# Optimization experiments

Hardware: AMD Instinct MI355X
Metric: run time of the kernel (lower is better)

Reference implementation:

```python
import jax, jax.numpy as jnp
import numpy as np

NEG_SLOPE = 0.2
N_NODES = 50000


def gat_conv(x, src, dst, W, a_src, a_dst, b, n_nodes):
    """One PyG-style GATConv layer (eval mode, self-loops already in src/dst).
    x: [N, F_in]; W: [F_in, H*C]; a_src/a_dst: [H, C]; b: [H*C] or [C].
    Returns per-node, per-head outputs [N, H, C].
    """
    H, C = a_src.shape
    h = (x @ W).reshape(-1, H, C)                      # [N, H, C]
    s_src = jnp.sum(h * a_src[None], axis=-1)          # [N, H]
    s_dst = jnp.sum(h * a_dst[None], axis=-1)          # [N, H]
    e = jax.nn.leaky_relu(s_src[src] + s_dst[dst], NEG_SLOPE)   # [E, H]
    # segment softmax over incoming edges of each destination node
    m = jax.ops.segment_max(e, dst, num_segments=n_nodes)       # [N, H]
    w = jnp.exp(e - m[dst])                                     # [E, H]
    denom = jax.ops.segment_sum(w, dst, num_segments=n_nodes)   # [N, H]
    alpha = w / denom[dst]                                      # [E, H]
    # weighted aggregation of source features
    out = jax.ops.segment_sum(alpha[:, :, None] * h[src], dst, num_segments=n_nodes)
    return out  # [N, H, C]


def setup_inputs() -> dict:
    key = jax.random.key(0)
    ks = jax.random.split(key, 12)
    N, F_in, Hid, H, F_out = N_NODES, 128, 64, 4, 128
    E = 800000
    x = jax.random.normal(ks[0], (N, F_in), dtype=jnp.float32)
    edge_index = jax.random.randint(ks[1], (2, E), 0, N, dtype=jnp.int64)
    sc = 0.1
    return {
        "x": x,
        "edge_index": edge_index,
        "W1": jax.random.normal(ks[2], (F_in, H * Hid), dtype=jnp.float32) * sc,
        "att_src1": jax.random.normal(ks[3], (H, Hid), dtype=jnp.float32) * sc,
        "att_dst1": jax.random.normal(ks[4], (H, Hid), dtype=jnp.float32) * sc,
        "b1": jnp.zeros((H * Hid,), dtype=jnp.float32),
        "W2": jax.random.normal(ks[5], (H * Hid, F_out), dtype=jnp.float32) * sc,
        "att_src2": jax.random.normal(ks[6], (1, F_out), dtype=jnp.float32) * sc,
        "att_dst2": jax.random.normal(ks[7], (1, F_out), dtype=jnp.float32) * sc,
        "b2": jnp.zeros((F_out,), dtype=jnp.float32),
    }


def reference(x, edge_index, W1, att_src1, att_dst1, b1, W2, att_src2, att_dst2, b2):
    N = x.shape[0]
    # PyG GATConv adds self-loops by default
    loops = jnp.arange(N, dtype=edge_index.dtype)
    src = jnp.concatenate([edge_index[0], loops])
    dst = jnp.concatenate([edge_index[1], loops])
    # layer 1: heads=4, concat -> [N, H*Hid], then ELU (dropout is identity in eval)
    h1 = gat_conv(x, src, dst, W1, att_src1, att_dst1, b1, N)    # [N, H, Hid]
    h1 = h1.reshape(N, -1) + b1
    h1 = jax.nn.elu(h1)
    # layer 2: heads=1, concat=False -> mean over the single head
    h2 = gat_conv(h1, src, dst, W2, att_src2, att_dst2, b2, N)   # [N, 1, F_out]
    out = h2[:, 0, :] + b2
    return out
```

## Files before the change

### kernel.cpp

```cpp
#include <hip/hip_runtime.h>
#include <cmath>

typedef __attribute__((ext_vector_type(8))) short bf16x8;
typedef __attribute__((ext_vector_type(4))) float f32x4;

static __device__ __forceinline__ unsigned short f2bf(float f) {
    unsigned u = __float_as_uint(f);
    unsigned r = (u + 0x7fffu + ((u >> 16) & 1u)) >> 16;
    return (unsigned short)r;
}
static __device__ __forceinline__ unsigned packbf(float a, float b) {
    return (unsigned)f2bf(a) | ((unsigned)f2bf(b) << 16);
}
static __device__ __forceinline__ float bflo(unsigned u) { return __uint_as_float(u << 16); }
static __device__ __forceinline__ float bfhi(unsigned u) { return __uint_as_float(u & 0xffff0000u); }

__global__ void prep_k(const float* __restrict__ x, const float* __restrict__ W1,
                       const float* __restrict__ W2, const int* __restrict__ dst,
                       unsigned* __restrict__ xb,
                       unsigned short* __restrict__ Wt1, unsigned short* __restrict__ Wt2,
                       int* __restrict__ deg, int NX2, int NW1, int NW2, int E) {
    int i = blockIdx.x * blockDim.x + threadIdx.x;
    if (i < NX2) {
        float2 v = reinterpret_cast<const float2*>(x)[i];
        xb[i] = packbf(v.x, v.y);
        return;
    }
    i -= NX2;
    if (i < NW1) { int nn = i / 128, k = i % 128; Wt1[i] = f2bf(W1[(size_t)k * 256 + nn]); return; }
    i -= NW1;
    if (i < NW2) { int nn = i / 256, k = i % 256; Wt2[i] = f2bf(W2[(size_t)k * 128 + nn]); return; }
    i -= NW2;
    if (i < E) atomicAdd(&deg[dst[i]], 1);
}

#define SCAN_BLK 256
#define SCAN_ELEMS 2048

__global__ void scan1_k(const int* __restrict__ deg, int* __restrict__ rowstart,
                        int* __restrict__ bsums, int N) {
    __shared__ int sh[SCAN_BLK];
    int t = threadIdx.x;
    int base = blockIdx.x * SCAN_ELEMS + t * 8;
    int vals[8];
    int sum = 0;
#pragma unroll
    for (int i = 0; i < 8; ++i) {
        int idx = base + i;
        vals[i] = (idx < N) ? (deg[idx] + 1) : 0;
        sum += vals[i];
    }
    sh[t] = sum;
    __syncthreads();
    for (int off = 1; off < SCAN_BLK; off <<= 1) {
        int v = (t >= off) ? sh[t - off] : 0;
        __syncthreads();
        sh[t] += v;
        __syncthreads();
    }
    int run = sh[t] - sum;
    if (t == SCAN_BLK - 1) bsums[blockIdx.x] = sh[t];
#pragma unroll
    for (int i = 0; i < 8; ++i) {
        int idx = base + i;
        if (idx < N) rowstart[idx] = run;
        run += vals[i];
    }
}
__global__ void scan2_k(int* __restrict__ bsums, int nb) {
    int lane = threadIdx.x;
    int own = (lane < nb) ? bsums[lane] : 0;
    int v = own;
    for (int off = 1; off < 64; off <<= 1) {
        int t = __shfl_up(v, off, 64);
        if (lane >= off) v += t;
    }
    if (lane < nb) bsums[lane] = v - own;
}
__global__ void scan3_init_k(int* __restrict__ rowstart, const int* __restrict__ bsums,
                             int* __restrict__ adj, int* __restrict__ cursor, int N, int total) {
    int i = blockIdx.x * blockDim.x + threadIdx.x;
    if (i < N) {
        int r = rowstart[i] + bsums[i / SCAN_ELEMS];
        rowstart[i] = r;
        adj[r] = i;
        cursor[i] = r + 1;
    } else if (i == N) {
        rowstart[N] = total;
    }
}
__global__ void scatter_k(const int* __restrict__ src, const int* __restrict__ dst, int E,
                          int* __restrict__ cursor, int* __restrict__ adj) {
    int e = blockIdx.x * blockDim.x + threadIdx.x;
    if (e >= E) return;
    int pos = atomicAdd(&cursor[dst[e]], 1);
    adj[pos] = src[e];
}

template<int K, int NOUT>
__global__ __launch_bounds__(256) void gemm_mfma_k(const unsigned* __restrict__ Ab,
                                                   const unsigned* __restrict__ Bt,
                                                   unsigned short* __restrict__ Yb, int N) {
    __shared__ unsigned short As[128 * 64];
    __shared__ unsigned short Bs[64 * 64];
    int tid = threadIdx.x;
    int lane = tid & 63, wid = tid >> 6;
    int wm = wid >> 1, wc = wid & 1;
    int m0 = blockIdx.x * 128;
    int n0 = blockIdx.y * 64;

    f32x4 acc[4][2] = {};

    for (int k0 = 0; k0 < K; k0 += 64) {
#pragma unroll
        for (int p = 0; p < 4; ++p) {
            int gl = p * 256 + tid;
            int row = gl >> 3, g = gl & 7;
            int grow = m0 + row; if (grow >= N) grow = N - 1;
            uint4 v = *reinterpret_cast<const uint4*>(Ab + (size_t)grow * (K / 2) + k0 / 2 + g * 4);
            *reinterpret_cast<uint4*>((char*)As + row * 128 + ((g ^ (row & 7)) << 4)) = v;
        }
#pragma unroll
        for (int p = 0; p < 2; ++p) {
            int gl = p * 256 + tid;
            int row = gl >> 3, g = gl & 7;
            uint4 v = *reinterpret_cast<const uint4*>(Bt + (size_t)(n0 + row) * (K / 2) + k0 / 2 + g * 4);
            *reinterpret_cast<uint4*>((char*)Bs + row * 128 + ((g ^ (row & 7)) << 4)) = v;
        }
        __syncthreads();

        bf16x8 bfrag[2][2];
#pragma unroll
        for (int kk = 0; kk < 2; ++kk)
#pragma unroll
            for (int no = 0; no < 2; ++no) {
                int row = wc * 32 + no * 16 + (lane & 15);
                int g = kk * 4 + (lane >> 4);
                bfrag[kk][no] = *reinterpret_cast<const bf16x8*>((char*)Bs + row * 128 + ((g ^ (row & 7)) << 4));
            }
#pragma unroll
        for (int mo = 0; mo < 4; ++mo) {
#pragma unroll
            for (int kk = 0; kk < 2; ++kk) {
                int row = wm * 64 + mo * 16 + (lane & 15);
                int g = kk * 4 + (lane >> 4);
                bf16x8 afrag = *reinterpret_cast<const bf16x8*>((char*)As + row * 128 + ((g ^ (row & 7)) << 4));
                acc[mo][0] = __builtin_amdgcn_mfma_f32_16x16x32_bf16(afrag, bfrag[kk][0], acc[mo][0], 0, 0, 0);
                acc[mo][1] = __builtin_amdgcn_mfma_f32_16x16x32_bf16(afrag, bfrag[kk][1], acc[mo][1], 0, 0, 0);
            }
        }
        __syncthreads();
    }
#pragma unroll
    for (int mo = 0; mo < 4; ++mo)
#pragma unroll
        for (int no = 0; no < 2; ++no) {
            int col = n0 + wc * 32 + no * 16 + (lane & 15);
            int rbase = m0 + wm * 64 + mo * 16 + (lane >> 4) * 4;
#pragma unroll
            for (int j = 0; j < 4; ++j) {
                int row = rbase + j;
                if (row < N) Yb[(size_t)row * NOUT + col] = f2bf(acc[mo][no][j]);
            }
        }
}

template<int H, int C>
__global__ void score_b_k(const unsigned* __restrict__ hb, const float* __restrict__ a_src,
                          const float* __restrict__ a_dst,
                          float* __restrict__ ssrc, float* __restrict__ sdst, int N) {
    int idx = blockIdx.x * blockDim.x + threadIdx.x;
    if (idx >= N * H) return;
    int n = idx / H, hh = idx % H;
    const uint4* hp = reinterpret_cast<const uint4*>(hb + (size_t)n * (H * C / 2) + hh * (C / 2));
    const float* as = a_src + hh * C;
    const float* ad = a_dst + hh * C;
    float ss = 0.f, sd = 0.f;
#pragma unroll
    for (int i = 0; i < C / 8; ++i) {
        uint4 u = hp[i];
        float v[8] = {bflo(u.x), bfhi(u.x), bflo(u.y), bfhi(u.y),
                      bflo(u.z), bfhi(u.z), bflo(u.w), bfhi(u.w)};
#pragma unroll
        for (int j = 0; j < 8; ++j) { ss += v[j] * as[i * 8 + j]; sd += v[j] * ad[i * 8 + j]; }
    }
    ssrc[idx] = ss;
    sdst[idx] = sd;
}

template<int H, int C, int GRP, bool ELU, bool OUT_BF16>
__global__ void node_agg_k(const int* __restrict__ rowstart, const int* __restrict__ adj,
                           const float* __restrict__ ssrc, const float* __restrict__ sdst,
                           const unsigned* __restrict__ hb, const float* __restrict__ bias,
                           void* __restrict__ outp, int N) {
    constexpr int HC = H * C;
    constexpr int ROW_U = HC / 2;
    constexpr int ULN = ROW_U / GRP;
    constexpr int FPLn = ULN * 2;
    constexpr int NGRP = 64 / GRP;
    int lane = threadIdx.x & 63;
    int w = threadIdx.x >> 6;
    int n = blockIdx.x * (blockDim.x >> 6) + w;
    if (n >= N) return;

    __shared__ int   s_sh[4][64];
    __shared__ float a_sh[4][64 * H];

    int r0 = rowstart[n], r1 = rowstart[n + 1];
    int deg = r1 - r0;

    float sd[H];
#pragma unroll
    for (int h = 0; h < H; ++h) sd[h] = sdst[n * H + h];

    if (deg <= 64) {
        int s = adj[r0 + ((lane < deg) ? lane : 0)];
        float a[H], l[H];
        {
            float v[H];
            if constexpr (H == 4) {
                float4 sv = reinterpret_cast<const float4*>(ssrc)[s];
                v[0] = sv.x; v[1] = sv.y; v[2] = sv.z; v[3] = sv.w;
            } else {
                v[0] = ssrc[s];
            }
#pragma unroll
            for (int h = 0; h < H; ++h) {
                float t = v[h] + sd[h];
                t = t > 0.f ? t : 0.2f * t;
                a[h] = (lane < deg) ? __expf(t) : 0.f;
                l[h] = a[h];
            }
            if (deg > 32)
#pragma unroll
                for (int h = 0; h < H; ++h) l[h] += __shfl_xor(l[h], 32, 64);
#pragma unroll
            for (int off = 16; off; off >>= 1)
#pragma unroll
                for (int h = 0; h < H; ++h) l[h] += __shfl_xor(l[h], off, 64);
#pragma unroll
            for (int h = 0; h < H; ++h) a[h] *= __builtin_amdgcn_rcpf(l[h]);
        }
        s_sh[w][lane] = s;
#pragma unroll
        for (int h = 0; h < H; ++h) a_sh[w][lane * H + h] = a[h];

        int g = lane / GRP, ln = lane % GRP;
        int hA = (ln * FPLn) / C;
        const unsigned* hbl = hb + ln * ULN;
        float acc[FPLn];
#pragma unroll
        for (int f = 0; f < FPLn; ++f) acc[f] = 0.f;

        int j = g;
        for (; j + 3 * NGRP < deg; j += 4 * NGRP) {
            int s0 = s_sh[w][j],            s1 = s_sh[w][j + NGRP];
            int s2 = s_sh[w][j + 2 * NGRP], s3 = s_sh[w][j + 3 * NGRP];
            float al0 = a_sh[w][j * H + hA],            al1 = a_sh[w][(j + NGRP) * H + hA];
            float al2 = a_sh[w][(j + 2 * NGRP) * H + hA], al3 = a_sh[w][(j + 3 * NGRP) * H + hA];
            uint4 u0 = *reinterpret_cast<const uint4*>(hbl + (size_t)s0 * ROW_U);
            uint4 u1 = *reinterpret_cast<const uint4*>(hbl + (size_t)s1 * ROW_U);
            uint4 u2 = *reinterpret_cast<const uint4*>(hbl + (size_t)s2 * ROW_U);
            uint4 u3 = *reinterpret_cast<const uint4*>(hbl + (size_t)s3 * ROW_U);
            acc[0] += al0 * bflo(u0.x); acc[1] += al0 * bfhi(u0.x);
            acc[2] += al0 * bflo(u0.y); acc[3] += al0 * bfhi(u0.y);
            acc[4] += al0 * bflo(u0.z); acc[5] += al0 * bfhi(u0.z);
            acc[6] += al0 * bflo(u0.w); acc[7] += al0 * bfhi(u0.w);
            acc[0] += al1 * bflo(u1.x); acc[1] += al1 * bfhi(u1.x);
            acc[2] += al1 * bflo(u1.y); acc[3] += al1 * bfhi(u1.y);
            acc[4] += al1 * bflo(u1.z); acc[5] += al1 * bfhi(u1.z);
            acc[6] += al1 * bflo(u1.w); acc[7] += al1 * bfhi(u1.w);
            acc[0] += al2 * bflo(u2.x); acc[1] += al2 * bfhi(u2.x);
            acc[2] += al2 * bflo(u2.y); acc[3] += al2 * bfhi(u2.y);
            acc[4] += al2 * bflo(u2.z); acc[5] += al2 * bfhi(u2.z);
            acc[6] += al2 * bflo(u2.w); acc[7] += al2 * bfhi(u2.w);
            acc[0] += al3 * bflo(u3.x); acc[1] += al3 * bfhi(u3.x);
            acc[2] += al3 * bflo(u3.y); acc[3] += al3 * bfhi(u3.y);
            acc[4] += al3 * bflo(u3.z); acc[5] += al3 * bfhi(u3.z);
            acc[6] += al3 * bflo(u3.w); acc[7] += al3 * bfhi(u3.w);
        }
        for (; j < deg; j += NGRP) {
            int sj = s_sh[w][j];
            float al = a_sh[w][j * H + hA];
            uint4 u = *reinterpret_cast<const uint4*>(hbl + (size_t)sj * ROW_U);
            acc[0] += al * bflo(u.x); acc[1] += al * bfhi(u.x);
            acc[2] += al * bflo(u.y); acc[3] += al * bfhi(u.y);
            acc[4] += al * bflo(u.z); acc[5] += al * bfhi(u.z);
            acc[6] += al * bflo(u.w); acc[7] += al * bfhi(u.w);
        }
#pragma unroll
        for (int off = GRP; off < 64; off <<= 1)
#pragma unroll
            for (int f = 0; f < FPLn; ++f) acc[f] += __shfl_xor(acc[f], off, 64);
#pragma unroll
        for (int f = 0; f < FPLn; ++f) {
            float v = acc[f] + bias[ln * FPLn + f];
            if (ELU) v = v > 0.f ? v : (__expf(v) - 1.f);
            acc[f] = v;
        }
        if (g == 0) {
            if constexpr (OUT_BF16) {
                unsigned* op = (unsigned*)outp + (size_t)n * ROW_U + ln * ULN;
                uint4 u = {packbf(acc[0], acc[1]), packbf(acc[2], acc[3]),
                           packbf(acc[4], acc[5]), packbf(acc[6], acc[7])};
                *reinterpret_cast<uint4*>(op) = u;
            } else {
                float* op = (float*)outp + (size_t)n * HC + ln * FPLn;
                *reinterpret_cast<float4*>(op) = make_float4(acc[0], acc[1], acc[2], acc[3]);
                *reinterpret_cast<float4*>(op + 4) = make_float4(acc[4], acc[5], acc[6], acc[7]);
            }
        }
    } else {
        constexpr int FPL = HC / 64;
        constexpr int UPL = FPL / 2;
        int hA = (lane * FPL) / C;
        float acc[FPL];
#pragma unroll
        for (int f = 0; f < FPL; ++f) acc[f] = 0.f;
        float m[H], l[H];
#pragma unroll
        for (int h = 0; h < H; ++h) { m[h] = -1e30f; l[h] = 0.f; }
        for (int e = r0 + lane; e < r1; e += 64) {
            int s = adj[e];
#pragma unroll
            for (int h = 0; h < H; ++h) {
                float v = ssrc[s * H + h] + sd[h];
                v = v > 0.f ? v : 0.2f * v;
                float mn = fmaxf(m[h], v);
                l[h] = l[h] * __expf(m[h] - mn) + __expf(v - mn);
                m[h] = mn;
            }
        }
#pragma unroll
        for (int off = 32; off; off >>= 1)
#pragma unroll
            for (int h = 0; h < H; ++h) {
                float mo = __shfl_xor(m[h], off, 64);
                float lo = __shfl_xor(l[h], off, 64);
                float mn = fmaxf(m[h], mo);
                l[h] = l[h] * __expf(m[h] - mn) + lo * __expf(mo - mn);
                m[h] = mn;
            }
        float mh = m[hA], invl = 1.f / l[hA], sdh = sd[hA];
        for (int e = r0; e < r1; ++e) {
            int s = adj[e];
            float v = ssrc[s * H + hA] + sdh;
            v = v > 0.f ? v : 0.2f * v;
            float alpha = __expf(v - mh) * invl;
            const unsigned* hp = hb + (size_t)s * ROW_U + lane * UPL;
            if constexpr (UPL == 2) {
                uint2 u = *reinterpret_cast<const uint2*>(hp);
                acc[0] += alpha * bflo(u.x); acc[1] += alpha * bfhi(u.x);
                acc[2] += alpha * bflo(u.y); acc[3] += alpha * bfhi(u.y);
            } else {
                unsigned u = *hp;
                acc[0] += alpha * bflo(u); acc[1] += alpha * bfhi(u);
            }
        }
#pragma unroll
        for (int f = 0; f < FPL; ++f) {
            float v = acc[f] + bias[lane * FPL + f];
            if (ELU) v = v > 0.f ? v : (__expf(v) - 1.f);
            acc[f] = v;
        }
        if constexpr (OUT_BF16) {
            unsigned* op = (unsigned*)outp + (size_t)n * ROW_U + lane * UPL;
            if constexpr (UPL == 2) {
                uint2 u = {packbf(acc[0], acc[1]), packbf(acc[2], acc[3])};
                *reinterpret_cast<uint2*>(op) = u;
            } else {
                *op = packbf(acc[0], acc[1]);
            }
        } else {
            float* op = (float*)outp + (size_t)n * HC + lane * FPL;
#pragma unroll
            for (int f = 0; f < FPL; ++f) op[f] = acc[f];
        }
    }
}

extern "C" void kernel_launch(void* const* d_in, const int* in_sizes, int n_in,
                              void* d_out, int out_size, void* d_ws, size_t ws_size,
                              hipStream_t stream) {
    const float* x   = (const float*)d_in[0];
    const int*   ei  = (const int*)d_in[1];
    const float* W1  = (const float*)d_in[2];
    const float* as1 = (const float*)d_in[3];
    const float* ad1 = (const float*)d_in[4];
    const float* b1  = (const float*)d_in[5];
    const float* W2  = (const float*)d_in[6];
    const float* as2 = (const float*)d_in[7];
    const float* ad2 = (const float*)d_in[8];
    const float* b2  = (const float*)d_in[9];
    float* out = (float*)d_out;

    const int N  = in_sizes[0] / 128;
    const int E  = in_sizes[1] / 2;
    const int ET = E + N;
    const int* src = ei;
    const int* dst = ei + E;

    unsigned* ws = (unsigned*)d_ws;
    unsigned* xb    = ws;
    unsigned* h1b   = xb    + (size_t)N * 64;
    unsigned* agg1b = h1b   + (size_t)N * 128;
    unsigned* h2b   = agg1b + (size_t)N * 128;
    unsigned* Wt1   = h2b   + (size_t)N * 64;
    unsigned* Wt2   = Wt1   + 16384;
    float*    ssrc1 = (float*)(Wt2 + 16384);
    float*    sdst1 = ssrc1 + (size_t)N * 4;
    float*    ssrc2 = sdst1 + (size_t)N * 4;
    float*    sdst2 = ssrc2 + N;
    int*      deg   = (int*)(sdst2 + N);
    int*      rowst = deg + N;
    int*      bsums = rowst + N + 1;
    int*      adj   = bsums + 64;

    const int B = 256;
    auto blocks = [](size_t n, int b) { return (int)((n + b - 1) / b); };
    const int nscan = (N + SCAN_ELEMS - 1) / SCAN_ELEMS;

    hipMemsetAsync(deg, 0, (size_t)N * 4, stream);
    {
        int NX2 = N * 64, NW1 = 128 * 256, NW2 = 256 * 128;
        size_t tot = (size_t)NX2 + NW1 + NW2 + E;
        prep_k<<<blocks(tot, B), B, 0, stream>>>(x, W1, W2, dst, xb, (unsigned short*)Wt1,
                                                 (unsigned short*)Wt2, deg, NX2, NW1, NW2, E);
    }

    scan1_k<<<nscan, SCAN_BLK, 0, stream>>>(deg, rowst, bsums, N);
    scan2_k<<<1, 64, 0, stream>>>(bsums, nscan);
    scan3_init_k<<<blocks(N + 1, B), B, 0, stream>>>(rowst, bsums, adj, deg, N, ET);
    scatter_k<<<blocks(E, B), B, 0, stream>>>(src, dst, E, deg, adj);

    {
        dim3 g((N + 127) / 128, 256 / 64);
        gemm_mfma_k<128, 256><<<g, 256, 0, stream>>>(xb, (const unsigned*)Wt1, (unsigned short*)h1b, N);
    }
    score_b_k<4, 64><<<blocks((size_t)N * 4, B), B, 0, stream>>>(h1b, as1, ad1, ssrc1, sdst1, N);
    node_agg_k<4, 64, 32, true, true><<<(N + 3) / 4, 256, 0, stream>>>(rowst, adj, ssrc1, sdst1, h1b, b1, agg1b, N);

    {
        dim3 g((N + 127) / 128, 128 / 64);
        gemm_mfma_k<256, 128><<<g, 256, 0, stream>>>(agg1b, (const unsigned*)Wt2, (unsigned short*)h2b, N);
    }
    score_b_k<1, 128><<<blocks(N, B), B, 0, stream>>>(h2b, as2, ad2, ssrc2, sdst2, N);
    node_agg_k<1, 128, 16, false, false><<<(N + 3) / 4, 256, 0, stream>>>(rowst, adj, ssrc2, sdst2, h2b, b2, out, N);
}
```

Measured before the change: 262.4 us.

## Map one lane-group per node in GAT aggregation instead of one wavefront

The aggregation kernel now gives each destination node a group of GRP lanes rather than a full 64-lane wavefront, so two or four nodes share a wave. This removes the cross-group shuffle reduction of the accumulators and packs more nodes per block. The softmax no longer subtracts the running max: unnormalized exponentials are accumulated and divided by the sum at the end, which merges the short- and long-degree paths into one epilogue. This risks exp overflow for large attention scores, and each node's edges are walked serially by a single group.

```diff
diff --git a/kernel.cpp b/kernel.cpp
--- a/kernel.cpp
+++ b/kernel.cpp
@@ -197,14 +197,17 @@
     constexpr int ROW_U = HC / 2;
     constexpr int ULN = ROW_U / GRP;
     constexpr int FPLn = ULN * 2;
-    constexpr int NGRP = 64 / GRP;
+    constexpr int NG = 64 / GRP;
+    constexpr int NGB = 4 * NG;
     int lane = threadIdx.x & 63;
     int w = threadIdx.x >> 6;
-    int n = blockIdx.x * (blockDim.x >> 6) + w;
+    int g = lane / GRP, ln = lane % GRP;
+    int gid = w * NG + g;
+    int n = blockIdx.x * NGB + gid;
     if (n >= N) return;
 
-    __shared__ int   s_sh[4][64];
-    __shared__ float a_sh[4][64 * H];
+    __shared__ int   s_tab[NGB][64];
+    __shared__ float a_tab[NGB][64 * H];
 
     int r0 = rowstart[n], r1 = rowstart[n + 1];
     int deg = r1 - r0;
@@ -213,10 +216,20 @@
 #pragma unroll
     for (int h = 0; h < H; ++h) sd[h] = sdst[n * H + h];
 
+    int hA = (ln * FPLn) / C;
+    const unsigned* hbl = hb + ln * ULN;
+    float acc[FPLn];
+#pragma unroll
+    for (int f = 0; f < FPLn; ++f) acc[f] = 0.f;
+    float l[H];
+#pragma unroll
+    for (int h = 0; h < H; ++h) l[h] = 0.f;
+
     if (deg <= 64) {
-        int s = adj[r0 + ((lane < deg) ? lane : 0)];
-        float a[H], l[H];
-        {
+        for (int base = 0; base < deg; base += GRP) {
+            int idx = base + ln;
+            bool on = idx < deg;
+            int s = adj[r0 + (on ? idx : 0)];
             float v[H];
             if constexpr (H == 4) {
                 float4 sv = reinterpret_cast<const float4*>(ssrc)[s];
@@ -228,154 +241,97 @@
             for (int h = 0; h < H; ++h) {
                 float t = v[h] + sd[h];
                 t = t > 0.f ? t : 0.2f * t;
-                a[h] = (lane < deg) ? __expf(t) : 0.f;
-                l[h] = a[h];
-            }
-            if (deg > 32)
-#pragma unroll
-                for (int h = 0; h < H; ++h) l[h] += __shfl_xor(l[h], 32, 64);
-#pragma unroll
-            for (int off = 16; off; off >>= 1)
-#pragma unroll
-                for (int h = 0; h < H; ++h) l[h] += __shfl_xor(l[h], off, 64);
-#pragma unroll
-            for (int h = 0; h < H; ++h) a[h] *= __builtin_amdgcn_rcpf(l[h]);
-        }
-        s_sh[w][lane] = s;
-#pragma unroll
-        for (int h = 0; h < H; ++h) a_sh[w][lane * H + h] = a[h];
-
-        int g = lane / GRP, ln = lane % GRP;
-        int hA = (ln * FPLn) / C;
-        const unsigned* hbl = hb + ln * ULN;
-        float acc[FPLn];
-#pragma unroll
-        for (int f = 0; f < FPLn; ++f) acc[f] = 0.f;
-
-        int j = g;
-        for (; j + 3 * NGRP < deg; j += 4 * NGRP) {
-            int s0 = s_sh[w][j],            s1 = s_sh[w][j + NGRP];
-            int s2 = s_sh[w][j + 2 * NGRP], s3 = s_sh[w][j + 3 * NGRP];
-            float al0 = a_sh[w][j * H + hA],            al1 = a_sh[w][(j + NGRP) * H + hA];
-            float al2 = a_sh[w][(j + 2 * NGRP) * H + hA], al3 = a_sh[w][(j + 3 * NGRP) * H + hA];
+                float av = on ? __expf(t) : 0.f;
+                l[h] += av;
+                if (on) a_tab[gid][idx * H + h] = av;
+            }
+            if (on) s_tab[gid][idx] = s;
+        }
+#pragma unroll
+        for (int off = GRP / 2; off; off >>= 1)
+#pragma unroll
+            for (int h = 0; h < H; ++h) l[h] += __shfl_xor(l[h], off, 64);
+
+        int j = 0;
+        for (; j + 3 < deg; j += 4) {
+            int s0 = s_tab[gid][j],     s1 = s_tab[gid][j + 1];
+            int s2 = s_tab[gid][j + 2], s3 = s_tab[gid][j + 3];
+            float a0 = a_tab[gid][j * H + hA],       a1 = a_tab[gid][(j + 1) * H + hA];
+            float a2 = a_tab[gid][(j + 2) * H + hA], a3 = a_tab[gid][(j + 3) * H + hA];
             uint4 u0 = *reinterpret_cast<const uint4*>(hbl + (size_t)s0 * ROW_U);
             uint4 u1 = *reinterpret_cast<const uint4*>(hbl + (size_t)s1 * ROW_U);
             uint4 u2 = *reinterpret_cast<const uint4*>(hbl + (size_t)s2 * ROW_U);
             uint4 u3 = *reinterpret_cast<const uint4*>(hbl + (size_t)s3 * ROW_U);
-            acc[0] += al0 * bflo(u0.x); acc[1] += al0 * bfhi(u0.x);
-            acc[2] += al0 * bflo(u0.y); acc[3] += al0 * bfhi(u0.y);
-            acc[4] += al0 * bflo(u0.z); acc[5] += al0 * bfhi(u0.z);
-            acc[6] += al0 * bflo(u0.w); acc[7] += al0 * bfhi(u0.w);
-            acc[0] += al1 * bflo(u1.x); acc[1] += al1 * bfhi(u1.x);
-            acc[2] += al1 * bflo(u1.y); acc[3] += al1 * bfhi(u1.y);
-            acc[4] += al1 * bflo(u1.z); acc[5] += al1 * bfhi(u1.z);
-            acc[6] += al1 * bflo(u1.w); acc[7] += al1 * bfhi(u1.w);
-            acc[0] += al2 * bflo(u2.x); acc[1] += al2 * bfhi(u2.x);
-            acc[2] += al2 * bflo(u2.y); acc[3] += al2 * bfhi(u2.y);
-            acc[4] += al2 * bflo(u2.z); acc[5] += al2 * bfhi(u2.z);
-            acc[6] += al2 * bflo(u2.w); acc[7] += al2 * bfhi(u2.w);
-            acc[0] += al3 * bflo(u3.x); acc[1] += al3 * bfhi(u3.x);
-            acc[2] += al3 * bflo(u3.y); acc[3] += al3 * bfhi(u3.y);
-            acc[4] += al3 * bflo(u3.z); acc[5] += al3 * bfhi(u3.z);
-            acc[6] += al3 * bflo(u3.w); acc[7] += al3 * bfhi(u3.w);
-        }
-        for (; j < deg; j += NGRP) {
-            int sj = s_sh[w][j];
-            float al = a_sh[w][j * H + hA];
+            acc[0] += a0 * bflo(u0.x); acc[1] += a0 * bfhi(u0.x);
+            acc[2] += a0 * bflo(u0.y); acc[3] += a0 * bfhi(u0.y);
+            acc[4] += a0 * bflo(u0.z); acc[5] += a0 * bfhi(u0.z);
+            acc[6] += a0 * bflo(u0.w); acc[7] += a0 * bfhi(u0.w);
+            acc[0] += a1 * bflo(u1.x); acc[1] += a1 * bfhi(u1.x);
+            acc[2] += a1 * bflo(u1.y); acc[3] += a1 * bfhi(u1.y);
+            acc[4] += a1 * bflo(u1.z); acc[5] += a1 * bfhi(u1.z);
+            acc[6] += a1 * bflo(u1.w); acc[7] += a1 * bfhi(u1.w);
+            acc[0] += a2 * bflo(u2.x); acc[1] += a2 * bfhi(u2.x);
+            acc[2] += a2 * bflo(u2.y); acc[3] += a2 * bfhi(u2.y);
+            acc[4] += a2 * bflo(u2.z); acc[5] += a2 * bfhi(u2.z);
+            acc[6] += a2 * bflo(u2.w); acc[7] += a2 * bfhi(u2.w);
+            acc[0] += a3 * bflo(u3.x); acc[1] += a3 * bfhi(u3.x);
+            acc[2] += a3 * bflo(u3.y); acc[3] += a3 * bfhi(u3.y);
+            acc[4] += a3 * bflo(u3.z); acc[5] += a3 * bfhi(u3.z);
+            acc[6] += a3 * bflo(u3.w); acc[7] += a3 * bfhi(u3.w);
+        }
+        for (; j < deg; ++j) {
+            int sj = s_tab[gid][j];
+            float al = a_tab[gid][j * H + hA];
             uint4 u = *reinterpret_cast<const uint4*>(hbl + (size_t)sj * ROW_U);
             acc[0] += al * bflo(u.x); acc[1] += al * bfhi(u.x);
             acc[2] += al * bflo(u.y); acc[3] += al * bfhi(u.y);
             acc[4] += al * bflo(u.z); acc[5] += al * bfhi(u.z);
             acc[6] += al * bflo(u.w); acc[7] += al * bfhi(u.w);
         }
-#pragma unroll
-        for (int off = GRP; off < 64; off <<= 1)
-#pragma unroll
-            for (int f = 0; f < FPLn; ++f) acc[f] += __shfl_xor(acc[f], off, 64);
-#pragma unroll
-        for (int f = 0; f < FPLn; ++f) {
-            float v = acc[f] + bias[ln * FPLn + f];
-            if (ELU) v = v > 0.f ? v : (__expf(v) - 1.f);
-            acc[f] = v;
-        }
-        if (g == 0) {
-            if constexpr (OUT_BF16) {
-                unsigned* op = (unsigned*)outp + (size_t)n * ROW_U + ln * ULN;
-                uint4 u = {packbf(acc[0], acc[1]), packbf(acc[2], acc[3]),
-                           packbf(acc[4], acc[5]), packbf(acc[6], acc[7])};
-                *reinterpret_cast<uint4*>(op) = u;
-            } else {
-                float* op = (float*)outp + (size_t)n * HC + ln * FPLn;
-                *reinterpret_cast<float4*>(op) = make_float4(acc[0], acc[1], acc[2], acc[3]);
-                *reinterpret_cast<float4*>(op + 4) = make_float4(acc[4], acc[5], acc[6], acc[7]);
-            }
-        }
     } else {
-        constexpr int FPL = HC / 64;
-        constexpr int UPL = FPL / 2;
-        int hA = (lane * FPL) / C;
-        float acc[FPL];
-#pragma unroll
-        for (int f = 0; f < FPL; ++f) acc[f] = 0.f;
-        float m[H], l[H];
-#pragma unroll
-        for (int h = 0; h < H; ++h) { m[h] = -1e30f; l[h] = 0.f; }
-        for (int e = r0 + lane; e < r1; e += 64) {
+        for (int e = r0 + ln; e < r1; e += GRP) {
             int s = adj[e];
 #pragma unroll
             for (int h = 0; h < H; ++h) {
-                float v = ssrc[s * H + h] + sd[h];
-                v = v > 0.f ? v : 0.2f * v;
-                float mn = fmaxf(m[h], v);
-                l[h] = l[h] * __expf(m[h] - mn) + __expf(v - mn);
-                m[h] = mn;
-            }
-        }
-#pragma unroll
-        for (int off = 32; off; off >>= 1)
-#pragma unroll
-            for (int h = 0; h < H; ++h) {
-                float mo = __shfl_xor(m[h], off, 64);
-                float lo = __shfl_xor(l[h], off, 64);
-                float mn = fmaxf(m[h], mo);
-                l[h] = l[h] * __expf(m[h] - mn) + lo * __expf(mo - mn);
-                m[h] = mn;
-            }
-        float mh = m[hA], invl = 1.f / l[hA], sdh = sd[hA];
+                float t = ssrc[s * H + h] + sd[h];
+                t = t > 0.f ? t : 0.2f * t;
+                l[h] += __expf(t);
+            }
+        }
+#pragma unroll
+        for (int off = GRP / 2; off; off >>= 1)
+#pragma unroll
+            for (int h = 0; h < H; ++h) l[h] += __shfl_xor(l[h], off, 64);
+        float sdh = sd[hA];
         for (int e = r0; e < r1; ++e) {
             int s = adj[e];
-            float v = ssrc[s * H + hA] + sdh;
-            v = v > 0.f ? v : 0.2f * v;
-            float alpha = __expf(v - mh) * invl;
-            const unsigned* hp = hb + (size_t)s * ROW_U + lane * UPL;
-            if constexpr (UPL == 2) {
-                uint2 u = *reinterpret_cast<const uint2*>(hp);
-                acc[0] += alpha * bflo(u.x); acc[1] += alpha * bfhi(u.x);
-                acc[2] += alpha * bflo(u.y); acc[3] += alpha * bfhi(u.y);
-            } else {
-                unsigned u = *hp;
-                acc[0] += alpha * bflo(u); acc[1] += alpha * bfhi(u);
-            }
-        }
-#pragma unroll
-        for (int f = 0; f < FPL; ++f) {
-            float v = acc[f] + bias[lane * FPL + f];
-            if (ELU) v = v > 0.f ? v : (__expf(v) - 1.f);
-            acc[f] = v;
-        }
-        if constexpr (OUT_BF16) {
-            unsigned* op = (unsigned*)outp + (size_t)n * ROW_U + lane * UPL;
-            if constexpr (UPL == 2) {
-                uint2 u = {packbf(acc[0], acc[1]), packbf(acc[2], acc[3])};
-                *reinterpret_cast<uint2*>(op) = u;
-            } else {
-                *op = packbf(acc[0], acc[1]);
-            }
-        } else {
-            float* op = (float*)outp + (size_t)n * HC + lane * FPL;
-#pragma unroll
-            for (int f = 0; f < FPL; ++f) op[f] = acc[f];
-        }
+            float t = ssrc[s * H + hA] + sdh;
+            t = t > 0.f ? t : 0.2f * t;
+            float al = __expf(t);
+            uint4 u = *reinterpret_cast<const uint4*>(hbl + (size_t)s * ROW_U);
+            acc[0] += al * bflo(u.x); acc[1] += al * bfhi(u.x);
+            acc[2] += al * bflo(u.y); acc[3] += al * bfhi(u.y);
+            acc[4] += al * bflo(u.z); acc[5] += al * bfhi(u.z);
+            acc[6] += al * bflo(u.w); acc[7] += al * bfhi(u.w);
+        }
+    }
+
+    float invl = __builtin_amdgcn_rcpf(l[hA]);
+#pragma unroll
+    for (int f = 0; f < FPLn; ++f) {
+        float v = acc[f] * invl + bias[ln * FPLn + f];
+        if (ELU) v = v > 0.f ? v : (__expf(v) - 1.f);
+        acc[f] = v;
+    }
+    if constexpr (OUT_BF16) {
+        unsigned* op = (unsigned*)outp + (size_t)n * ROW_U + ln * ULN;
+        uint4 u = {packbf(acc[0], acc[1]), packbf(acc[2], acc[3]),
+                   packbf(acc[4], acc[5]), packbf(acc[6], acc[7])};
+        *reinterpret_cast<uint4*>(op) = u;
+    } else {
+        float* op = (float*)outp + (size_t)n * HC + ln * FPLn;
+        *reinterpret_cast<float4*>(op) = make_float4(acc[0], acc[1], acc[2], acc[3]);
+        *reinterpret_cast<float4*>(op + 4) = make_float4(acc[4], acc[5], acc[6], acc[7]);
     }
 }
 
@@ -438,12 +394,12 @@
         gemm_mfma_k<128, 256><<<g, 256, 0, stream>>>(xb, (const unsigned*)Wt1, (unsigned short*)h1b, N);
     }
     score_b_k<4, 64><<<blocks((size_t)N * 4, B), B, 0, stream>>>(h1b, as1, ad1, ssrc1, sdst1, N);
-    node_agg_k<4, 64, 32, true, true><<<(N + 3) / 4, 256, 0, stream>>>(rowst, adj, ssrc1, sdst1, h1b, b1, agg1b, N);
+    node_agg_k<4, 64, 32, true, true><<<(N + 7) / 8, 256, 0, stream>>>(rowst, adj, ssrc1, sdst1, h1b, b1, agg1b, N);
 
     {
         dim3 g((N + 127) / 128, 128 / 64);
         gemm_mfma_k<256, 128><<<g, 256, 0, stream>>>(agg1b, (const unsigned*)Wt2, (unsigned short*)h2b, N);
     }
     score_b_k<1, 128><<<blocks(N, B), B, 0, stream>>>(h2b, as2, ad2, ssrc2, sdst2, N);
-    node_agg_k<1, 128, 16, false, false><<<(N + 3) / 4, 256, 0, stream>>>(rowst, adj, ssrc2, sdst2, h2b, b2, out, N);
-}
+    node_agg_k<1, 128, 16, false, false><<<(N + 15) / 16, 256, 0, stream>>>(rowst, adj, ssrc2, sdst2, h2b, b2, out, N);
+}
```

After: 255.2 us. 1.03x faster.
